# Optimization experiments

Hardware: AMD Instinct MI355X
Metric: run time of the kernel (lower is better)

## Reference

```python
import jax, jax.numpy as jnp
import numpy as np


def _conv1x1(x, w, b):
    # x: [B,Cin,H,W], w: [Cout,Cin], b: [Cout]
    return jnp.einsum('bchw,oc->bohw', x, w) + b[None, :, None, None]


def setup_inputs() -> dict:
    key = jax.random.key(0)
    ks = jax.random.split(key, 9)
    C, Cb = 256, 128
    B, H, W = 8, 32, 32
    s_in = 1.0 / np.sqrt(C)
    s_bn = 1.0 / np.sqrt(Cb)
    return {
        'x': jax.random.normal(ks[0], (B, C, H, W), dtype=jnp.float32),
        'theta_w': jax.random.uniform(ks[1], (Cb, C), jnp.float32, -s_in, s_in),
        'theta_b': jax.random.uniform(ks[2], (Cb,), jnp.float32, -s_in, s_in),
        'phi_w': jax.random.uniform(ks[3], (Cb, C), jnp.float32, -s_in, s_in),
        'phi_b': jax.random.uniform(ks[4], (Cb,), jnp.float32, -s_in, s_in),
        'g_w': jax.random.uniform(ks[5], (Cb, C), jnp.float32, -s_in, s_in),
        'g_b': jax.random.uniform(ks[6], (Cb,), jnp.float32, -s_in, s_in),
        'W_w': jax.random.uniform(ks[7], (C, Cb), jnp.float32, -s_bn, s_bn),
        'W_b': jax.random.uniform(ks[8], (C,), jnp.float32, -s_bn, s_bn),
    }


def reference(x, theta_w, theta_b, phi_w, phi_b, g_w, g_b, W_w, W_b):
    B, C, H, Wd = x.shape
    Cb = theta_w.shape[0]
    theta = _conv1x1(x, theta_w, theta_b).reshape(-1, Cb)      # [N, Cb] (row-major, as torch)
    phi = _conv1x1(x, phi_w, phi_b).reshape(Cb, -1)            # [Cb, N]
    g = _conv1x1(x, g_w, g_b).reshape(-1, Cb)                  # [N, Cb]
    attn = jax.nn.softmax(theta @ phi, axis=1)                 # [N, N] global attention
    out = (attn @ g).reshape(B, -1, H, Wd)                     # [B, Cb, H, W]
    return _conv1x1(out, W_w, W_b) + x
```

## Files before the change

kernel.cpp:

```cpp
#include <hip/hip_runtime.h>

typedef unsigned short u16;
typedef __attribute__((ext_vector_type(8))) short short8;
typedef __attribute__((ext_vector_type(4))) float f32x4;

__device__ __forceinline__ u16 f2bf(float f){
  union { float f; unsigned u; } v; v.f = f;
  unsigned u = v.u;
  u += 0x7fffu + ((u >> 16) & 1u);
  return (u16)(u >> 16);
}
__device__ __forceinline__ float bf2f(u16 h){
  union { unsigned u; float f; } v; v.u = ((unsigned)h) << 16;
  return v.f;
}

__global__ __launch_bounds__(256) void wcast_kernel(
    const float* __restrict__ tw, const float* __restrict__ pw,
    const float* __restrict__ gw, u16* __restrict__ Wall)
{
  int i = blockIdx.x*256 + threadIdx.x;
  const float* src = (i < 8192) ? tw : (i < 16384) ? pw : gw;
  int off = (i & 8191) * 4;
  float4 v = *(const float4*)(src + off);
  ushort4 o;
  o.x = f2bf(v.x); o.y = f2bf(v.y); o.z = f2bf(v.z); o.w = f2bf(v.w);
  *(ushort4*)(Wall + (size_t)i*4) = o;
}

__global__ __launch_bounds__(256) void xcast_kernel(
    const float* __restrict__ x, u16* __restrict__ XT)
{
  __shared__ float tile[64][69];
  const int b = blockIdx.z, c0 = blockIdx.y*64, hw0 = blockIdx.x*64;
  const int t = threadIdx.x;
  {
    int r = t >> 2, cs = (t & 3) * 16;
    const float* s = x + (size_t)(b*256 + c0 + r)*1024 + hw0 + cs;
    #pragma unroll
    for (int i=0;i<4;i++)
      *(float4*)&tile[r][cs + i*4] = *(const float4*)(s + i*4);
  }
  __syncthreads();
  {
    int hr = t >> 2, cc = (t & 3) * 16;
    __align__(16) u16 tmp[16];
    #pragma unroll
    for (int i=0;i<16;i++) tmp[i] = f2bf(tile[cc + i][hr]);
    u16* d = XT + (size_t)(b*1024 + hw0 + hr)*256 + c0 + cc;
    *(uint4*)d     = *(uint4*)&tmp[0];
    *(uint4*)(d+8) = *(uint4*)&tmp[8];
  }
}

__global__ __launch_bounds__(256, 2) void proj_mfma_kernel(
    const u16* __restrict__ XT, const u16* __restrict__ Wall,
    const float* __restrict__ tb, const float* __restrict__ pb,
    const float* __restrict__ gb,
    u16* __restrict__ T, u16* __restrict__ PHI, u16* __restrict__ G)
{
  __shared__ __align__(16) u16 Ws[128][136];
  __shared__ __align__(16) u16 Xs[128][136];
  const int proj = blockIdx.x, qg = blockIdx.y;
  const int b = qg >> 3, hw0 = (qg & 7) * 128;
  const int q0 = qg * 128;
  const u16* Wsrc = Wall + (size_t)proj * 32768;
  const float* bias = (proj==0) ? tb : (proj==1) ? pb : gb;
  u16* out          = (proj==0) ? T  : (proj==1) ? PHI : G;
  const int t = threadIdx.x;
  const int wave = t >> 6, lane = t & 63;
  const int quad = lane >> 4, n16 = lane & 15;

  f32x4 acc[8][2];
  #pragma unroll
  for (int mt=0;mt<8;mt++)
    #pragma unroll
    for (int nt=0;nt<2;nt++){ f32x4 z = {0.f,0.f,0.f,0.f}; acc[mt][nt] = z; }

  for (int c0 = 0; c0 < 256; c0 += 128){
    __syncthreads();
    {
      int row = t >> 1, cb = (t & 1) * 64;
      const u16* s1 = Wsrc + (size_t)row*256 + c0 + cb;
      #pragma unroll
      for (int i=0;i<8;i++)
        *(uint4*)&Ws[row][cb + i*8] = *(const uint4*)(s1 + i*8);
      const u16* s2 = XT + (size_t)(q0 + row)*256 + c0 + cb;
      #pragma unroll
      for (int i=0;i<8;i++)
        *(uint4*)&Xs[row][cb + i*8] = *(const uint4*)(s2 + i*8);
    }
    __syncthreads();
    #pragma unroll
    for (int kc=0; kc<4; kc++){
      short8 xf[2];
      #pragma unroll
      for (int nt=0;nt<2;nt++)
        xf[nt] = *(const short8*)&Xs[wave*32 + nt*16 + n16][kc*32 + quad*8];
      #pragma unroll
      for (int mt=0;mt<8;mt++){
        short8 wf = *(const short8*)&Ws[mt*16 + n16][kc*32 + quad*8];
        #pragma unroll
        for (int nt=0;nt<2;nt++)
          acc[mt][nt] = __builtin_amdgcn_mfma_f32_16x16x32_bf16(wf, xf[nt], acc[mt][nt], 0, 0, 0);
      }
    }
  }
  #pragma unroll
  for (int mt=0;mt<8;mt++){
    float4 bv = *(const float4*)&bias[mt*16 + quad*4];
    float bb[4] = {bv.x, bv.y, bv.z, bv.w};
    #pragma unroll
    for (int nt=0;nt<2;nt++)
      #pragma unroll
      for (int r=0;r<4;r++)
        out[(size_t)b*131072 + (size_t)(mt*16 + quad*4 + r)*1024
            + hw0 + wave*32 + nt*16 + n16] = f2bf(acc[mt][nt][r] + bb[r]);
  }
}

__global__ __launch_bounds__(256) void transpose_bf_kernel(
    const u16* __restrict__ src, u16* __restrict__ dst, int R, int C)
{
  __shared__ u16 tile[64][72];
  const int t = threadIdx.x;
  const int c0 = blockIdx.x*64, r0 = blockIdx.y*64;
  {
    int rr = t >> 2, cs = (t & 3) * 16;
    const u16* s = src + (size_t)(r0+rr)*C + c0 + cs;
    uint4 a0 = *(const uint4*)s;
    uint4 a1 = *(const uint4*)(s+8);
    *(uint4*)&tile[rr][cs]   = a0;
    *(uint4*)&tile[rr][cs+8] = a1;
  }
  __syncthreads();
  {
    int cc = t >> 2, rs = (t & 3) * 16;
    __align__(16) u16 tmp[16];
    #pragma unroll
    for (int i=0;i<16;i++) tmp[i] = tile[rs+i][cc];
    u16* d = dst + (size_t)(c0+cc)*R + r0 + rs;
    *(uint4*)d     = *(uint4*)&tmp[0];
    *(uint4*)(d+8) = *(uint4*)&tmp[8];
  }
}

__global__ __launch_bounds__(256, 2) void attn_kernel(
    const u16* __restrict__ Tq, const u16* __restrict__ Kk,
    const u16* __restrict__ Vt, u16* __restrict__ Opart,
    float* __restrict__ lpart)
{
  __shared__ __align__(16) u16 Ks[64][136];
  __shared__ __align__(16) u16 Vs[128][72];
  __shared__ __align__(16) u16 Pall[4][4608];

  const int t = threadIdx.x;
  const int wave = t >> 6, lane = t & 63;
  const int quad = lane >> 4, n16 = lane & 15;
  const int s  = blockIdx.x & 15;
  const int qg = blockIdx.x >> 4;
  const int q0 = qg*256 + wave*64;
  u16* Pw = Pall[wave];
  u16*   Os = Opart + (size_t)s * 1048576;
  float* ls = lpart + (size_t)s * 8192;

  short8 qa[4][4];
  #pragma unroll
  for (int mt=0;mt<4;mt++)
    #pragma unroll
    for (int kc=0;kc<4;kc++)
      qa[mt][kc] = *(const short8*)(Tq + (size_t)(q0 + mt*16 + n16)*128 + kc*32 + quad*8);

  f32x4 o[4][8];
  float lp[4];
  #pragma unroll
  for (int mt=0;mt<4;mt++){
    #pragma unroll
    for (int dt=0;dt<8;dt++){ f32x4 z = {0.f,0.f,0.f,0.f}; o[mt][dt] = z; }
    lp[mt] = 0.f;
  }

  const int krow = t >> 2, kcs = (t & 3) * 32;
  const int vrow = t >> 1, vcs = (t & 1) * 32;
  const int wmask = n16 & 14;

  for (int kt = s*8; kt < s*8 + 8; kt++){
    const int key0 = kt * 64;
    __syncthreads();
    #pragma unroll
    for (int i=0;i<4;i++)
      *(uint4*)&Ks[krow][kcs + i*8] =
        *(const uint4*)(Kk + (size_t)(key0 + krow)*128 + kcs + i*8);
    #pragma unroll
    for (int i=0;i<4;i++)
      *(uint4*)&Vs[vrow][vcs + i*8] =
        *(const uint4*)(Vt + (size_t)vrow*8192 + key0 + vcs + i*8);
    __syncthreads();

    #pragma unroll
    for (int ntk=0; ntk<4; ntk++){
      short8 kf[4];
      #pragma unroll
      for (int kc=0;kc<4;kc++)
        kf[kc] = *(const short8*)&Ks[ntk*16 + n16][kc*32 + quad*8];
      #pragma unroll
      for (int mtq=0;mtq<4;mtq++){
        f32x4 sa = {0.f,0.f,0.f,0.f};
        #pragma unroll
        for (int kc=0;kc<4;kc++)
          sa = __builtin_amdgcn_mfma_f32_16x16x32_bf16(kf[kc], qa[mtq][kc], sa, 0, 0, 0);
        u16 pb[4];
        #pragma unroll
        for (int r=0;r<4;r++){
          float pe = exp2f(sa[r] * 1.4426950408889634f);
          lp[mtq] += pe;
          pb[r] = f2bf(pe);
        }
        uint2 pk;
        pk.x = ((unsigned)pb[1] << 16) | pb[0];
        pk.y = ((unsigned)pb[3] << 16) | pb[2];
        *(uint2*)(Pw + (mtq*16 + n16)*72 + (((ntk*4 + quad) ^ wmask) << 2)) = pk;
      }
    }

    __builtin_amdgcn_s_waitcnt(0xC07F);

    #pragma unroll
    for (int kb=0; kb<2; kb++){
      short8 pf[4];
      #pragma unroll
      for (int mtq=0;mtq<4;mtq++)
        pf[mtq] = *(const short8*)(Pw + (mtq*16 + n16)*72 + (((kb*8 + quad*2) ^ wmask) << 2));
      #pragma unroll
      for (int dt=0; dt<8; dt++){
        short8 vfd = *(const short8*)&Vs[dt*16 + n16][kb*32 + quad*8];
        #pragma unroll
        for (int mtq=0;mtq<4;mtq++)
          o[mtq][dt] = __builtin_amdgcn_mfma_f32_16x16x32_bf16(pf[mtq], vfd, o[mtq][dt], 0, 0, 0);
      }
    }
  }

  float l[4];
  #pragma unroll
  for (int mt=0;mt<4;mt++){
    float v = lp[mt];
    v += __shfl_xor(v, 16, 64);
    v += __shfl_xor(v, 32, 64);
    l[mt] = v;
  }

  #pragma unroll
  for (int mt=0;mt<4;mt++){
    #pragma unroll
    for (int r=0;r<4;r++){
      __align__(16) u16 tmp[8];
      #pragma unroll
      for (int dt=0;dt<8;dt++) tmp[dt] = f2bf(o[mt][dt][r]);
      *(uint4*)(Os + (size_t)(q0 + mt*16 + quad*4 + r)*128 + n16*8) = *(uint4*)tmp;
    }
    if (lane < 16)
      ls[q0 + mt*16 + lane] = l[mt];
  }
}

__global__ __launch_bounds__(256) void merge_o_kernel(
    const u16* __restrict__ Opart, const float* __restrict__ lpart, int S,
    u16* __restrict__ OmT)
{
  __shared__ u16 Tm[64][136];
  __shared__ float lrow[64];
  const int t = threadIdx.x;
  const int row0 = blockIdx.x * 64;
  const int b  = row0 >> 10;
  const int j0 = (row0 >> 3) & 127;

  if (t < 64){
    float v = 0.f;
    for (int sp=0; sp<S; sp++) v += lpart[sp*8192 + row0 + t];
    lrow[t] = 1.0f / v;
  }

  const int rl = t >> 2;
  const int cb = (t & 3) * 32;
  float acc[32];
  #pragma unroll
  for (int j=0;j<32;j++) acc[j] = 0.f;
  for (int sp=0; sp<S; sp++){
    const u16* p = Opart + (size_t)sp*1048576 + (size_t)(row0 + rl)*128 + cb;
    #pragma unroll
    for (int q=0;q<4;q++){
      ushort4 v = *(const ushort4*)(p + q*8);
      ushort4 w = *(const ushort4*)(p + q*8 + 4);
      acc[q*8+0] += bf2f(v.x); acc[q*8+1] += bf2f(v.y);
      acc[q*8+2] += bf2f(v.z); acc[q*8+3] += bf2f(v.w);
      acc[q*8+4] += bf2f(w.x); acc[q*8+5] += bf2f(w.y);
      acc[q*8+6] += bf2f(w.z); acc[q*8+7] += bf2f(w.w);
    }
  }
  __syncthreads();
  const float inv = lrow[rl];
  #pragma unroll
  for (int j=0;j<32;j++){
    int cp = cb + j;
    int ch = (cp & 7)*16 + (cp >> 3);
    Tm[rl][ch] = f2bf(acc[j] * inv);
  }
  __syncthreads();
  {
    const int hwhi = t >> 5;
    const int chb  = (t & 31) * 4;
    #pragma unroll
    for (int c=0;c<4;c++){
      int ch = chb + c;
      __align__(16) u16 tmp[8];
      #pragma unroll
      for (int jl=0;jl<8;jl++) tmp[jl] = Tm[jl*8 + hwhi][ch];
      *(uint4*)(OmT + (size_t)(b*1024 + hwhi*128 + ch)*128 + j0) = *(uint4*)tmp;
    }
  }
}

__global__ __launch_bounds__(256, 2) void final_mfma_kernel(
    const float* __restrict__ Ww, const float* __restrict__ Wb,
    const u16* __restrict__ OmT, const float* __restrict__ x,
    float* __restrict__ outp)
{
  __shared__ __align__(16) u16 Ws[64][136];
  __shared__ __align__(16) u16 Os[128][136];
  const int co0 = blockIdx.x * 64, qg = blockIdx.y;
  const int b = qg >> 3, hw0 = (qg & 7) * 128;
  const int q0 = qg * 128;
  const int t = threadIdx.x;
  const int wave = t >> 6, lane = t & 63;
  const int quad = lane >> 4, n16 = lane & 15;

  {
    int row = t >> 2, cbf = (t & 3) * 32;
    const float* sw = Ww + (size_t)(co0 + row)*128 + cbf;
    #pragma unroll
    for (int i=0;i<8;i++){
      float4 v = *(const float4*)(sw + i*4);
      u16* d = &Ws[row][cbf + i*4];
      d[0]=f2bf(v.x); d[1]=f2bf(v.y); d[2]=f2bf(v.z); d[3]=f2bf(v.w);
    }
  }
  {
    int row = t >> 1, cb = (t & 1) * 64;
    const u16* so = OmT + (size_t)(q0 + row)*128 + cb;
    #pragma unroll
    for (int i=0;i<8;i++)
      *(uint4*)&Os[row][cb + i*8] = *(const uint4*)(so + i*8);
  }
  __syncthreads();

  f32x4 acc[4][2];
  #pragma unroll
  for (int mt=0;mt<4;mt++)
    #pragma unroll
    for (int nt=0;nt<2;nt++){ f32x4 z = {0.f,0.f,0.f,0.f}; acc[mt][nt] = z; }

  #pragma unroll
  for (int kc=0; kc<4; kc++){
    short8 xf[2];
    #pragma unroll
    for (int nt=0;nt<2;nt++)
      xf[nt] = *(const short8*)&Os[wave*32 + nt*16 + n16][kc*32 + quad*8];
    #pragma unroll
    for (int mt=0;mt<4;mt++){
      short8 wf = *(const short8*)&Ws[mt*16 + n16][kc*32 + quad*8];
      #pragma unroll
      for (int nt=0;nt<2;nt++)
        acc[mt][nt] = __builtin_amdgcn_mfma_f32_16x16x32_bf16(wf, xf[nt], acc[mt][nt], 0, 0, 0);
    }
  }

  #pragma unroll
  for (int mt=0;mt<4;mt++){
    float4 bv = *(const float4*)&Wb[co0 + mt*16 + quad*4];
    float bb[4] = {bv.x, bv.y, bv.z, bv.w};
    #pragma unroll
    for (int nt=0;nt<2;nt++)
      #pragma unroll
      for (int r=0;r<4;r++){
        size_t idx = (size_t)b*262144 + (size_t)(co0 + mt*16 + quad*4 + r)*1024
                   + hw0 + wave*32 + nt*16 + n16;
        outp[idx] = acc[mt][nt][r] + bb[r] + x[idx];
      }
  }
}

extern "C" void kernel_launch(void* const* d_in, const int* in_sizes, int n_in,
                              void* d_out, int out_size, void* d_ws, size_t ws_size,
                              hipStream_t stream)
{
  (void)in_sizes; (void)n_in; (void)out_size; (void)ws_size;
  const float* x  = (const float*)d_in[0];
  const float* tw = (const float*)d_in[1];
  const float* tb = (const float*)d_in[2];
  const float* pw = (const float*)d_in[3];
  const float* pb = (const float*)d_in[4];
  const float* gw = (const float*)d_in[5];
  const float* gb = (const float*)d_in[6];
  const float* Ww = (const float*)d_in[7];
  const float* Wb = (const float*)d_in[8];
  float* outp = (float*)d_out;

  char* ws = (char*)d_ws;
  const size_t MB = 1u << 20;
  u16*   Tbf   = (u16*)(ws);
  u16*   PHIbf = (u16*)(ws + 2*MB);
  u16*   Gbf   = (u16*)(ws + 4*MB);
  u16*   Kbf   = (u16*)(ws + 6*MB);
  u16*   VTbf  = (u16*)(ws + 8*MB);
  u16*   Opart = (u16*)(ws + 10*MB);
  u16*   XT    = (u16*)(ws + 10*MB);
  u16*   Wall  = (u16*)(ws + 14*MB);
  float* lpart = (float*)(ws + 2*MB);
  u16*   OmT   = (u16*)(ws + 4*MB);

  wcast_kernel<<<dim3(96), 256, 0, stream>>>(tw, pw, gw, Wall);
  xcast_kernel<<<dim3(16, 4, 8), 256, 0, stream>>>(x, XT);
  proj_mfma_kernel<<<dim3(3, 64), 256, 0, stream>>>(XT, Wall, tb, pb, gb,
                                                    Tbf, PHIbf, Gbf);
  transpose_bf_kernel<<<dim3(128, 2), 256, 0, stream>>>(PHIbf, Kbf, 128, 8192);
  transpose_bf_kernel<<<dim3(2, 128), 256, 0, stream>>>(Gbf, VTbf, 8192, 128);
  attn_kernel<<<dim3(512), 256, 0, stream>>>(Tbf, Kbf, VTbf, Opart, lpart);
  merge_o_kernel<<<dim3(128), 256, 0, stream>>>(Opart, lpart, 16, OmT);
  final_mfma_kernel<<<dim3(4, 64), 256, 0, stream>>>(Ww, Wb, OmT, x, outp);
}
```

Before: 187.9 us.

## Load K/V tiles directly to LDS with swizzle and fold log2e into theta

Replaces the register-staged K and V tile copies in the attention kernel with global_load_lds direct-to-LDS loads into an XOR-swizzled unpadded layout, and updates the MFMA fragment reads to match. The log2(e) factor moves into the theta projection epilogue so the softmax uses the raw hardware exp2. It also raises wave priority around the PV MFMA block. This cuts VGPR pressure and load instructions, but the direct LDS loads are followed by a full vmcnt(0) wait, so there is still no overlap between loading and compute.

```diff
diff --git a/kernel.cpp b/kernel.cpp
--- a/kernel.cpp
+++ b/kernel.cpp
@@ -13,6 +13,11 @@
 __device__ __forceinline__ float bf2f(u16 h){
   union { unsigned u; float f; } v; v.u = ((unsigned)h) << 16;
   return v.f;
+}
+__device__ __forceinline__ void gload16(const u16* g, u16* l){
+  __builtin_amdgcn_global_load_lds(
+      (const __attribute__((address_space(1))) unsigned int*)g,
+      (__attribute__((address_space(3))) unsigned int*)l, 16, 0, 0);
 }
 
 __global__ __launch_bounds__(256) void wcast_kernel(
@@ -67,6 +72,7 @@
   const u16* Wsrc = Wall + (size_t)proj * 32768;
   const float* bias = (proj==0) ? tb : (proj==1) ? pb : gb;
   u16* out          = (proj==0) ? T  : (proj==1) ? PHI : G;
+  const float scale = (proj==0) ? 1.4426950408889634f : 1.0f;
   const int t = threadIdx.x;
   const int wave = t >> 6, lane = t & 63;
   const int quad = lane >> 4, n16 = lane & 15;
@@ -115,7 +121,7 @@
       #pragma unroll
       for (int r=0;r<4;r++)
         out[(size_t)b*131072 + (size_t)(mt*16 + quad*4 + r)*1024
-            + hw0 + wave*32 + nt*16 + n16] = f2bf(acc[mt][nt][r] + bb[r]);
+            + hw0 + wave*32 + nt*16 + n16] = f2bf((acc[mt][nt][r] + bb[r]) * scale);
   }
 }
 
@@ -150,8 +156,8 @@
     const u16* __restrict__ Vt, u16* __restrict__ Opart,
     float* __restrict__ lpart)
 {
-  __shared__ __align__(16) u16 Ks[64][136];
-  __shared__ __align__(16) u16 Vs[128][72];
+  __shared__ __align__(16) u16 Ks[8192];
+  __shared__ __align__(16) u16 Vs[8192];
   __shared__ __align__(16) u16 Pall[4][4608];
 
   const int t = threadIdx.x;
@@ -180,21 +186,32 @@
     lp[mt] = 0.f;
   }
 
-  const int krow = t >> 2, kcs = (t & 3) * 32;
-  const int vrow = t >> 1, vcs = (t & 1) * 32;
+  const int ck0   = wave * 4;
+  const int rk_l  = lane >> 4;
+  const int rv_l  = lane >> 3;
+  const int cbk_l = (lane & 15) * 16;
+  const int cbv_l = (lane & 7) * 16;
   const int wmask = n16 & 14;
+  const int swz   = (n16 & 7) << 4;
 
   for (int kt = s*8; kt < s*8 + 8; kt++){
     const int key0 = kt * 64;
     __syncthreads();
     #pragma unroll
-    for (int i=0;i<4;i++)
-      *(uint4*)&Ks[krow][kcs + i*8] =
-        *(const uint4*)(Kk + (size_t)(key0 + krow)*128 + kcs + i*8);
-    #pragma unroll
-    for (int i=0;i<4;i++)
-      *(uint4*)&Vs[vrow][vcs + i*8] =
-        *(const uint4*)(Vt + (size_t)vrow*8192 + key0 + vcs + i*8);
+    for (int i=0;i<4;i++){
+      const int ck = ck0 + i;
+      const int rk = ck*4 + rk_l;
+      gload16(Kk + (size_t)(key0 + rk)*128 + ((cbk_l ^ ((rk & 7) << 4)) >> 1),
+              &Ks[ck*512]);
+    }
+    #pragma unroll
+    for (int i=0;i<4;i++){
+      const int ck = ck0 + i;
+      const int rv = ck*8 + rv_l;
+      gload16(Vt + (size_t)rv*8192 + key0 + ((cbv_l ^ ((rv & 7) << 4)) >> 1),
+              &Vs[ck*512]);
+    }
+    asm volatile("s_waitcnt vmcnt(0)" ::: "memory");
     __syncthreads();
 
     #pragma unroll
@@ -202,7 +219,8 @@
       short8 kf[4];
       #pragma unroll
       for (int kc=0;kc<4;kc++)
-        kf[kc] = *(const short8*)&Ks[ntk*16 + n16][kc*32 + quad*8];
+        kf[kc] = *(const short8*)((const char*)Ks
+                   + ((ntk*16 + n16) << 8) + ((kc*64 + quad*16) ^ swz));
       #pragma unroll
       for (int mtq=0;mtq<4;mtq++){
         f32x4 sa = {0.f,0.f,0.f,0.f};
@@ -212,7 +230,7 @@
         u16 pb[4];
         #pragma unroll
         for (int r=0;r<4;r++){
-          float pe = exp2f(sa[r] * 1.4426950408889634f);
+          float pe = __builtin_amdgcn_exp2f(sa[r]);
           lp[mtq] += pe;
           pb[r] = f2bf(pe);
         }
@@ -231,13 +249,16 @@
       #pragma unroll
       for (int mtq=0;mtq<4;mtq++)
         pf[mtq] = *(const short8*)(Pw + (mtq*16 + n16)*72 + (((kb*8 + quad*2) ^ wmask) << 2));
+      __builtin_amdgcn_s_setprio(1);
       #pragma unroll
       for (int dt=0; dt<8; dt++){
-        short8 vfd = *(const short8*)&Vs[dt*16 + n16][kb*32 + quad*8];
+        short8 vfd = *(const short8*)((const char*)Vs
+                       + ((dt*16 + n16) << 7) + ((kb*64 + quad*16) ^ swz));
         #pragma unroll
         for (int mtq=0;mtq<4;mtq++)
           o[mtq][dt] = __builtin_amdgcn_mfma_f32_16x16x32_bf16(pf[mtq], vfd, o[mtq][dt], 0, 0, 0);
       }
+      __builtin_amdgcn_s_setprio(0);
     }
   }
 
```

Measured after the change: 197.5 us. +5.1%, slower.
